# Kernel optimization log

Measured on AMD Instinct MI355X. Metric: run time of the kernel, lower is better.

## Reference

```python
import jax, jax.numpy as jnp
import numpy as np

B, T, D, H, L, O = 256, 512, 64, 256, 2, 4


def _lstm_layer(x_tbd, W_ih, W_hh, b_ih, b_hh):
    """x_tbd: (T, B, D_in) -> hidden sequence (T, B, H). PyTorch gate order i,f,g,o."""
    Bb = x_tbd.shape[1]
    Hh = W_hh.shape[1]
    b = b_ih + b_hh
    # precompute input projections for all timesteps in one GEMM
    xW = jnp.einsum('tbd,gd->tbg', x_tbd, W_ih) + b  # (T, B, 4H)

    def step(carry, xw_t):
        h, c = carry
        gates = xw_t + h @ W_hh.T
        i, f, g, o = jnp.split(gates, 4, axis=-1)
        i = jax.nn.sigmoid(i)
        f = jax.nn.sigmoid(f)
        g = jnp.tanh(g)
        o = jax.nn.sigmoid(o)
        c = f * c + i * g
        h = o * jnp.tanh(c)
        return (h, c), h

    init = (jnp.zeros((Bb, Hh), x_tbd.dtype), jnp.zeros((Bb, Hh), x_tbd.dtype))
    _, hs = jax.lax.scan(step, init, xW)
    return hs


def setup_inputs() -> dict:
    key = jax.random.key(0)
    ks = jax.random.split(key, 11)
    s = 1.0 / np.sqrt(H)  # PyTorch LSTM init scale
    inp = {
        'x': jax.random.normal(ks[0], (B, T, D), dtype=jnp.float32),
        'W_ih0': jax.random.uniform(ks[1], (4 * H, D), minval=-s, maxval=s, dtype=jnp.float32),
        'W_hh0': jax.random.uniform(ks[2], (4 * H, H), minval=-s, maxval=s, dtype=jnp.float32),
        'b_ih0': jax.random.uniform(ks[3], (4 * H,), minval=-s, maxval=s, dtype=jnp.float32),
        'b_hh0': jax.random.uniform(ks[4], (4 * H,), minval=-s, maxval=s, dtype=jnp.float32),
        'W_ih1': jax.random.uniform(ks[5], (4 * H, H), minval=-s, maxval=s, dtype=jnp.float32),
        'W_hh1': jax.random.uniform(ks[6], (4 * H, H), minval=-s, maxval=s, dtype=jnp.float32),
        'b_ih1': jax.random.uniform(ks[7], (4 * H,), minval=-s, maxval=s, dtype=jnp.float32),
        'b_hh1': jax.random.uniform(ks[8], (4 * H,), minval=-s, maxval=s, dtype=jnp.float32),
        'fc_W': jax.random.uniform(ks[9], (O, H), minval=-s, maxval=s, dtype=jnp.float32),
        'fc_b': jax.random.uniform(ks[10], (O,), minval=-s, maxval=s, dtype=jnp.float32),
    }
    return inp


def reference(x, W_ih0, W_hh0, b_ih0, b_hh0, W_ih1, W_hh1, b_ih1, b_hh1, fc_W, fc_b):
    xt = jnp.transpose(x, (1, 0, 2))            # (T, B, D), batch_first -> time-major
    h1 = _lstm_layer(xt, W_ih0, W_hh0, b_ih0, b_hh0)   # (T, B, H)
    h2 = _lstm_layer(h1, W_ih1, W_hh1, b_ih1, b_hh1)   # (T, B, H)
    last = h2[-1]                                # out[:, -1, :] in batch_first layout
    return last @ fc_W.T + fc_b                  # (B, O)
```

## Files before the change

### kernel.cpp

```cpp
#include <hip/hip_runtime.h>


#define TT 512
#define HH 256
#define DD 64

typedef __attribute__((ext_vector_type(2))) _Float16 h2t;
typedef __attribute__((ext_vector_type(8))) _Float16 f16x8;
typedef __attribute__((ext_vector_type(4))) float f32x4;
typedef unsigned long long u64;
typedef unsigned u32;

__device__ __forceinline__ u32 pkh(float x, float y) {
    h2t h; h.x = (_Float16)x; h.y = (_Float16)y;
    return __builtin_bit_cast(u32, h);
}
__device__ __forceinline__ float sigf(float x) { return 1.f / (1.f + __expf(-x)); }
__device__ __forceinline__ float tanhf_(float x) {
    float e = __expf(2.f * x);
    return 1.f - 2.f / (e + 1.f);
}
__device__ __forceinline__ f16x8 ld8(const float* p) {
    float4 u = ((const float4*)p)[0];
    float4 v = ((const float4*)p)[1];
    f16x8 r = {(_Float16)u.x, (_Float16)u.y, (_Float16)u.z, (_Float16)u.w,
               (_Float16)v.x, (_Float16)v.y, (_Float16)v.z, (_Float16)v.w};
    return r;
}
__device__ __forceinline__ u32 ld32(const u32* p) {
    return __hip_atomic_load(p, __ATOMIC_RELAXED, __HIP_MEMORY_SCOPE_AGENT);
}
__device__ __forceinline__ void st32(u32* p, u32 v) {
    __hip_atomic_store(p, v, __ATOMIC_RELAXED, __HIP_MEMORY_SCOPE_AGENT);
}
__device__ __forceinline__ u64 ld64(const u64* p) {
    return __hip_atomic_load(p, __ATOMIC_RELAXED, __HIP_MEMORY_SCOPE_AGENT);
}
__device__ __forceinline__ void st64(u64* p, u64 v) {
    __hip_atomic_store(p, v, __ATOMIC_RELAXED, __HIP_MEMORY_SCOPE_AGENT);
}

__global__ __launch_bounds__(512, 2) void lstm_persist(
    const float* __restrict__ x,
    const float* __restrict__ Wih0, const float* __restrict__ Whh0,
    const float* __restrict__ bih0, const float* __restrict__ bhh0,
    const float* __restrict__ Wih1, const float* __restrict__ Whh1,
    const float* __restrict__ bih1, const float* __restrict__ bhh1,
    const float* __restrict__ fcW, const float* __restrict__ fcb,
    float* __restrict__ out,
    u64* h0ring, u64* h1ring, u32* cflagsA)
{
    __shared__ __align__(16) _Float16 sB[9216];
    __shared__ __align__(16) float part2[2][8][276];

    const int tid  = threadIdx.x;
    const int g    = blockIdx.x & 31;
    const int role = blockIdx.x >> 5;
    const bool isL1 = role >= 4;
    const int q = role & 3;
    const int batch0 = g * 8;
    u64* ring0 = h0ring + (size_t)g * 4096;
    u64* ring1 = h1ring + (size_t)g * 4096;
    u32* cflag = cflagsA + (size_t)g * 16;

    const int lane = tid & 63, w = tid >> 6;
    const int mw = w & 3, kh = w >> 2;
    const int bcol = lane & 15, kc = lane >> 4;

    const int R0 = mw * 256 + 64 * q + (lane & 15);
    const int R1 = R0 + 16, R2 = R0 + 32, R3 = R0 + 48;

#define DECL_TI(ti) f16x8 A##ti##_0={},A##ti##_1={},A##ti##_2={},A##ti##_3={}, \
                          A##ti##_4={},A##ti##_5={},A##ti##_6={},A##ti##_7={};
    DECL_TI(0) DECL_TI(1) DECL_TI(2) DECL_TI(3)
#undef DECL_TI

    if (isL1) {
#define LDA1(ti,j) { int k_ = (kh*8+(j))*32 + kc*8;                          \
        A##ti##_##j = ld8(k_ < 256 ? Wih1 + (size_t)R##ti*256 + k_           \
                                   : Whh1 + (size_t)R##ti*256 + (k_-256)); }
#define LDA1T(ti) LDA1(ti,0) LDA1(ti,1) LDA1(ti,2) LDA1(ti,3) \
                  LDA1(ti,4) LDA1(ti,5) LDA1(ti,6) LDA1(ti,7)
        LDA1T(0) LDA1T(1) LDA1T(2) LDA1T(3)
#undef LDA1T
#undef LDA1
    } else {
#define LDA0(ti,j) { int k_ = (kh*5+(j))*32 + kc*8;                          \
        A##ti##_##j = ld8(k_ < 64 ? Wih0 + (size_t)R##ti*64 + k_             \
                                  : Whh0 + (size_t)R##ti*256 + (k_-64)); }
#define LDA0T(ti) LDA0(ti,0) LDA0(ti,1) LDA0(ti,2) LDA0(ti,3) LDA0(ti,4)
        LDA0T(0) LDA0T(1) LDA0T(2) LDA0T(3)
#undef LDA0T
#undef LDA0
    }

    const float* bA = isL1 ? bih1 : bih0;
    const float* bB = isL1 ? bhh1 : bhh0;
    const float bz0 = bA[      64*q + lane] + bB[      64*q + lane];
    const float bz1 = bA[256 + 64*q + lane] + bB[256 + 64*q + lane];
    const float bz2 = bA[512 + 64*q + lane] + bB[512 + 64*q + lane];
    const float bz3 = bA[768 + 64*q + lane] + bB[768 + 64*q + lane];
    float cst = 0.f;

    u32* const sBu = (u32*)sB;
    for (int i = tid; i < 4608; i += 512) sBu[i] = 0;

    auto stage_next = [&](int snext) {
        const bool st0 = (!isL1) && (snext < TT);
        const bool st1 = isL1 && (snext >= 1) && (snext <= TT);
        if (!(st0 || st1)) return;
        {
            const int slot = (snext - 1) & 3;
            const u32 e0 = (u32)snext;
            const int base = isL1 ? 0 : 8;
#pragma unroll
            for (int pp = 0; pp < 2; ++pp) {
                int p = tid + pp * 512;
                int j = p >> 7, n = p & 127;
                const u64* a = ring0 + slot * 1024 + (n >> 5) * 256 + j * 32 + (n & 31);
                u64 v;
                do { v = ld64(a); } while ((u32)(v >> 32) != e0);
                sBu[(base + (n >> 2)) * 72 + j * 4 + (n & 3)] = (u32)v;
            }
        }
        if (isL1) {
            const int slot = (snext + 2) & 3;
            const u32 e1 = (snext >= 2) ? (u32)snext : 0u;
#pragma unroll
            for (int pp = 0; pp < 2; ++pp) {
                int p = tid + pp * 512;
                int j = p >> 7, n = p & 127;
                const u64* a = ring1 + slot * 1024 + (n >> 5) * 256 + j * 32 + (n & 31);
                u64 v;
                do { v = ld64(a); } while ((u32)(v >> 32) != e1);
                sBu[(32 + (n >> 2)) * 72 + j * 4 + (n & 3)] = (u32)v;
            }
        } else if (tid >= 256 && tid < 384) {
            int t2 = tid - 256, j = t2 >> 4, c = t2 & 15;
            float4 v = ((const float4*)(x + ((size_t)(batch0 + j) * TT + snext) * DD))[c];
            int bidx = (c >> 1) * 72 + j * 4 + (c & 1) * 2;
            sBu[bidx]     = pkh(v.x, v.y);
            sBu[bidx + 1] = pkh(v.z, v.w);
        }
    };
    stage_next(0);

    for (int s = 0; s <= TT; ++s) {
        __syncthreads();
        if (tid == 0) st32(&cflag[role], (u32)(s + 1));

        const bool act_ = isL1 ? (s >= 1) : (s < TT);

        u32 cpre = 0xFFFFFFFFu;
        if (act_ && lane < 8) cpre = ld32(&cflag[lane]);

        if (act_) {
            f32x4 C0 = {0,0,0,0}, C1 = {0,0,0,0}, C2 = {0,0,0,0}, C3 = {0,0,0,0};
#define MST(j, ktb) { const f16x8 Bf = *(const f16x8*)(sB + (((ktb)+(j))*4 + kc)*144 + bcol*8); \
            C0 = __builtin_amdgcn_mfma_f32_16x16x32_f16(A0_##j, Bf, C0, 0,0,0); \
            C1 = __builtin_amdgcn_mfma_f32_16x16x32_f16(A1_##j, Bf, C1, 0,0,0); \
            C2 = __builtin_amdgcn_mfma_f32_16x16x32_f16(A2_##j, Bf, C2, 0,0,0); \
            C3 = __builtin_amdgcn_mfma_f32_16x16x32_f16(A3_##j, Bf, C3, 0,0,0); }
            if (isL1) {
                const int ktb = kh * 8;
                MST(0,ktb) MST(1,ktb) MST(2,ktb) MST(3,ktb)
                MST(4,ktb) MST(5,ktb) MST(6,ktb) MST(7,ktb)
            } else {
                const int ktb = kh * 5;
                MST(0,ktb) MST(1,ktb) MST(2,ktb) MST(3,ktb) MST(4,ktb)
            }
#undef MST
            if (bcol < 8) {
                *(f32x4*)&part2[kh][bcol][mw*64 +  0 + kc*4] = C0;
                *(f32x4*)&part2[kh][bcol][mw*64 + 16 + kc*4] = C1;
                *(f32x4*)&part2[kh][bcol][mw*64 + 32 + kc*4] = C2;
                *(f32x4*)&part2[kh][bcol][mw*64 + 48 + kc*4] = C3;
            }
        }
        __syncthreads();

        if (act_) {
            float s0 = part2[0][w][      lane] + part2[1][w][      lane] + bz0;
            float s1 = part2[0][w][ 64 + lane] + part2[1][w][ 64 + lane] + bz1;
            float s2 = part2[0][w][128 + lane] + part2[1][w][128 + lane] + bz2;
            float s3 = part2[0][w][192 + lane] + part2[1][w][192 + lane] + bz3;
            float fi = sigf(s0), ff = sigf(s1), fg = tanhf_(s2), fo = sigf(s3);
            cst = ff * cst + fi * fg;
            float h = fo * tanhf_(cst);
            float hn = __shfl_down(h, 1);

            const int tgt = s - 2;
            while (!__all(lane >= 8 || (int)cpre >= tgt)) {
                __builtin_amdgcn_s_sleep(1);
                if (lane < 8) cpre = ld32(&cflag[lane]);
            }
            if (!(lane & 1)) {
                u64 v = ((u64)(u32)(s + 1) << 32) | (u64)pkh(h, hn);
                u64* dst = (isL1 ? ring1 + (size_t)((s - 1) & 3) * 1024
                                 : ring0 + (size_t)(s & 3) * 1024)
                           + q * 256 + w * 32 + (lane >> 1);
                st64(dst, v);
            }
        }

        stage_next(s + 1);
    }

    if (isL1 && q == 0) {
        const u32 ef = (u32)(TT + 1);
#pragma unroll
        for (int pp = 0; pp < 2; ++pp) {
            int p = tid + pp * 512;
            int j = p >> 7, n = p & 127;
            const u64* a = ring1 + 3 * 1024 + (n >> 5) * 256 + j * 32 + (n & 31);
            u64 v;
            do { v = ld64(a); } while ((u32)(v >> 32) != ef);
            sBu[j * 128 + n] = (u32)v;
        }
        __syncthreads();
        const int j = tid >> 6, l2 = tid & 63;
        const int o = l2 >> 4, kk = l2 & 15;
        float ssum = 0.f;
#pragma unroll
        for (int m = 0; m < 16; ++m) {
            int k = kk * 16 + m;
            ssum += (float)sB[j * 256 + k] * fcW[o * HH + k];
        }
#pragma unroll
        for (int off = 8; off; off >>= 1) ssum += __shfl_down(ssum, off);
        if (kk == 0) out[(batch0 + j) * 4 + o] = ssum + fcb[o];
    }
}

extern "C" void kernel_launch(void* const* d_in, const int* in_sizes, int n_in,
                              void* d_out, int out_size, void* d_ws, size_t ws_size,
                              hipStream_t stream)
{
    (void)in_sizes; (void)n_in; (void)out_size; (void)ws_size;
    const float* x    = (const float*)d_in[0];
    const float* Wih0 = (const float*)d_in[1];
    const float* Whh0 = (const float*)d_in[2];
    const float* bih0 = (const float*)d_in[3];
    const float* bhh0 = (const float*)d_in[4];
    const float* Wih1 = (const float*)d_in[5];
    const float* Whh1 = (const float*)d_in[6];
    const float* bih1 = (const float*)d_in[7];
    const float* bhh1 = (const float*)d_in[8];
    const float* fcW  = (const float*)d_in[9];
    const float* fcb  = (const float*)d_in[10];
    float* out = (float*)d_out;

    u64* h0ring = (u64*)d_ws;
    u64* h1ring = (u64*)((char*)d_ws + 1048576);
    u32* cflags = (u32*)((char*)d_ws + 2097152);

    hipMemsetAsync(d_ws, 0, 2097152 + 2048, stream);

    lstm_persist<<<dim3(256), dim3(512), 0, stream>>>(
        x, Wih0, Whh0, bih0, bhh0, Wih1, Whh1, bih1, bhh1, fcW, fcb, out,
        h0ring, h1ring, cflags);
}
```

Measured before the change: 1.278 ms.

## Split input projections into separate producer blocks and pipeline them ahead of recurrence

```diff
diff --git a/kernel.cpp b/kernel.cpp
--- a/kernel.cpp
+++ b/kernel.cpp
@@ -39,6 +39,10 @@
 __device__ __forceinline__ void st64(u64* p, u64 v) {
     __hip_atomic_store(p, v, __ATOMIC_RELAXED, __HIP_MEMORY_SCOPE_AGENT);
 }
+
+#define MFMA16(A, B, C) __builtin_amdgcn_mfma_f32_16x16x32_f16((A), (B), (C), 0, 0, 0)
+
+#define DECLF(ti) f16x8 A##ti##_0 = {}, A##ti##_1 = {}, A##ti##_2 = {}, A##ti##_3 = {};
 
 __global__ __launch_bounds__(512, 2) void lstm_persist(
     const float* __restrict__ x,
@@ -48,187 +52,267 @@
     const float* __restrict__ bih1, const float* __restrict__ bhh1,
     const float* __restrict__ fcW, const float* __restrict__ fcb,
     float* __restrict__ out,
-    u64* h0ring, u64* h1ring, u32* cflagsA)
+    u64* wsu, u32* cflagsA)
 {
-    __shared__ __align__(16) _Float16 sB[9216];
-    __shared__ __align__(16) float part2[2][8][276];
+    __shared__ __align__(16) char ldsraw[9216 + 33280];
+    _Float16* const sB16 = (_Float16*)ldsraw;
+    u32* const sBu = (u32*)ldsraw;
+    float (*const part2)[8][520] = (float(*)[8][520])(ldsraw + 9216);
+    float (*const p1)[1032] = (float(*)[1032])(ldsraw + 9216);
 
     const int tid  = threadIdx.x;
     const int g    = blockIdx.x & 31;
     const int role = blockIdx.x >> 5;
-    const bool isL1 = role >= 4;
-    const int q = role & 3;
     const int batch0 = g * 8;
-    u64* ring0 = h0ring + (size_t)g * 4096;
-    u64* ring1 = h1ring + (size_t)g * 4096;
-    u32* cflag = cflagsA + (size_t)g * 16;
+    u64* const h0ring = wsu + (size_t)g * 4096;
+    u64* const h1ring = wsu + 131072 + (size_t)g * 4096;
+    u64* const u0ring = wsu + 262144 + (size_t)g * 16384;
+    u64* const u1ring = wsu + 786432 + (size_t)g * 16384;
+    u32* const cflag  = cflagsA + (size_t)g * 16;
 
     const int lane = tid & 63, w = tid >> 6;
     const int mw = w & 3, kh = w >> 2;
     const int bcol = lane & 15, kc = lane >> 4;
 
-    const int R0 = mw * 256 + 64 * q + (lane & 15);
-    const int R1 = R0 + 16, R2 = R0 + 32, R3 = R0 + 48;
-
-#define DECL_TI(ti) f16x8 A##ti##_0={},A##ti##_1={},A##ti##_2={},A##ti##_3={}, \
-                          A##ti##_4={},A##ti##_5={},A##ti##_6={},A##ti##_7={};
-    DECL_TI(0) DECL_TI(1) DECL_TI(2) DECL_TI(3)
-#undef DECL_TI
-
-    if (isL1) {
-#define LDA1(ti,j) { int k_ = (kh*8+(j))*32 + kc*8;                          \
-        A##ti##_##j = ld8(k_ < 256 ? Wih1 + (size_t)R##ti*256 + k_           \
-                                   : Whh1 + (size_t)R##ti*256 + (k_-256)); }
-#define LDA1T(ti) LDA1(ti,0) LDA1(ti,1) LDA1(ti,2) LDA1(ti,3) \
-                  LDA1(ti,4) LDA1(ti,5) LDA1(ti,6) LDA1(ti,7)
-        LDA1T(0) LDA1T(1) LDA1T(2) LDA1T(3)
-#undef LDA1T
-#undef LDA1
+    for (int i = tid; i < 2304; i += 512) sBu[i] = 0;
+    __syncthreads();
+
+    if (role < 4) {
+        const int hf = role & 1;
+        const bool L1 = role >= 2;
+        const float* const W = L1 ? Whh1 : Whh0;
+        u64* const hring = L1 ? h1ring : h0ring;
+        const u64* const uring = L1 ? u1ring : u0ring;
+        const int ng = L1 ? 1 : 3;
+        const int gfi = (lane == 0) ? (role ^ 1) : (3 + lane);
+
+        DECLF(0) DECLF(1) DECLF(2) DECLF(3) DECLF(4) DECLF(5) DECLF(6) DECLF(7)
+#define LREC(ti) { const int R_ = mw * 256 + hf * 128 + (ti) * 16 + (lane & 15);  \
+        const float* rw_ = W + (size_t)R_ * 256 + kh * 128 + kc * 8;              \
+        A##ti##_0 = ld8(rw_);      A##ti##_1 = ld8(rw_ + 32);                     \
+        A##ti##_2 = ld8(rw_ + 64); A##ti##_3 = ld8(rw_ + 96); }
+        LREC(0) LREC(1) LREC(2) LREC(3) LREC(4) LREC(5) LREC(6) LREC(7)
+#undef LREC
+
+        const int j2 = w;
+        const int up = lane;
+        float c0_ = 0.f, c1_ = 0.f;
+
+        for (int s = 0; s < TT; ++s) {
+            if (tid == 0) st32(&cflag[role], (u32)(s + 1));
+            u32 cp = 0;
+            if (lane < ng) cp = ld32(&cflag[gfi]);
+
+            {
+                const f16x8 B0_ = *(const f16x8*)(sB16 + (kh*16 + 0*4 + kc)*144 + bcol*8);
+                const f16x8 B1_ = *(const f16x8*)(sB16 + (kh*16 + 1*4 + kc)*144 + bcol*8);
+                const f16x8 B2_ = *(const f16x8*)(sB16 + (kh*16 + 2*4 + kc)*144 + bcol*8);
+                const f16x8 B3_ = *(const f16x8*)(sB16 + (kh*16 + 3*4 + kc)*144 + bcol*8);
+#define MTR(ti) { f32x4 C_ = {0,0,0,0};                                           \
+                C_ = MFMA16(A##ti##_0, B0_, C_); C_ = MFMA16(A##ti##_1, B1_, C_); \
+                C_ = MFMA16(A##ti##_2, B2_, C_); C_ = MFMA16(A##ti##_3, B3_, C_); \
+                if (bcol < 8)                                                     \
+                    *(f32x4*)&part2[kh][bcol][mw*128 + (ti)*16 + kc*4] = C_; }
+                MTR(0) MTR(1) MTR(2) MTR(3) MTR(4) MTR(5) MTR(6) MTR(7)
+#undef MTR
+            }
+            __syncthreads();
+
+            const u32 eu = (u32)(s + 1);
+            const u64* ub_ = uring + (size_t)(s & 3) * 4096 + (size_t)j2 * 512
+                             + hf * 64 + up;
+            const u64 *ua0 = ub_, *ua1 = ub_ + 128, *ua2 = ub_ + 256, *ua3 = ub_ + 384;
+            u64 v0 = ld64(ua0), v1 = ld64(ua1), v2 = ld64(ua2), v3 = ld64(ua3);
+            for (;;) {
+                bool k0 = ((u32)(v0 >> 32) == eu), k1 = ((u32)(v1 >> 32) == eu);
+                bool k2 = ((u32)(v2 >> 32) == eu), k3 = ((u32)(v3 >> 32) == eu);
+                if (k0 & k1 & k2 & k3) break;
+                if (!k0) v0 = ld64(ua0);
+                if (!k1) v1 = ld64(ua1);
+                if (!k2) v2 = ld64(ua2);
+                if (!k3) v3 = ld64(ua3);
+            }
+            float e0, o0, e1, o1, e2, o2, e3, o3;
+#define GG(gi, vv) { const float2 xa = *(const float2*)&part2[0][j2][(gi)*128 + 2*up]; \
+            const float2 xb = *(const float2*)&part2[1][j2][(gi)*128 + 2*up];          \
+            const h2t uh = __builtin_bit_cast(h2t, (u32)(vv));                         \
+            e##gi = xa.x + xb.x + (float)uh.x; o##gi = xa.y + xb.y + (float)uh.y; }
+            GG(0, v0) GG(1, v1) GG(2, v2) GG(3, v3)
+#undef GG
+            {
+                float ie = sigf(e0), fe = sigf(e1), ge = tanhf_(e2), oe = sigf(e3);
+                c0_ = fe * c0_ + ie * ge;
+                e0 = oe * tanhf_(c0_);
+            }
+            {
+                float io = sigf(o0), fo = sigf(o1), go = tanhf_(o2), oo = sigf(o3);
+                c1_ = fo * c1_ + io * go;
+                o0 = oo * tanhf_(c1_);
+            }
+            const u32 hw = pkh(e0, o0);
+
+            sBu[(hf*16 + (up >> 2)) * 72 + j2 * 4 + (up & 3)] = hw;
+
+            {
+                const int tgt = s - 2;
+                while (!__all(lane >= ng || (int)cp >= tgt)) {
+                    __builtin_amdgcn_s_sleep(1);
+                    if (lane < ng) cp = ld32(&cflag[gfi]);
+                }
+            }
+            st64(hring + (size_t)(s & 3) * 1024 + (size_t)hf * 512 + j2 * 64 + up,
+                 ((u64)eu << 32) | (u64)hw);
+
+            {
+                const u64* pa_ = hring + (size_t)(s & 3) * 1024
+                                 + (size_t)(1 - hf) * 512 + j2 * 64 + up;
+                u64 pv = ld64(pa_);
+                while ((u32)(pv >> 32) != eu) pv = ld64(pa_);
+                sBu[((1 - hf)*16 + (up >> 2)) * 72 + j2 * 4 + (up & 3)] = (u32)pv;
+            }
+            __syncthreads();
+        }
+
+        if (role == 2) {
+            const int j = tid >> 6, l2 = tid & 63;
+            const int o = l2 >> 4, kk = l2 & 15;
+            float ssum = 0.f;
+#pragma unroll
+            for (int m = 0; m < 16; ++m) {
+                int k = kk * 16 + m;
+                ssum += (float)sB16[(k >> 3) * 144 + j * 8 + (k & 7)] * fcW[o * HH + k];
+            }
+#pragma unroll
+            for (int off = 8; off; off >>= 1) ssum += __shfl_down(ssum, off);
+            if (kk == 0) out[(batch0 + j) * 4 + o] = ssum + fcb[o];
+        }
+    } else if (role < 6) {
+        const int rh = role - 4;
+        DECLF(0) DECLF(1) DECLF(2) DECLF(3) DECLF(4) DECLF(5) DECLF(6) DECLF(7)
+#define LU1(ti) { const int R_ = rh * 512 + mw * 128 + (ti) * 16 + (lane & 15);   \
+        const float* rw_ = Wih1 + (size_t)R_ * 256 + kh * 128 + kc * 8;           \
+        A##ti##_0 = ld8(rw_);      A##ti##_1 = ld8(rw_ + 32);                     \
+        A##ti##_2 = ld8(rw_ + 64); A##ti##_3 = ld8(rw_ + 96); }
+        LU1(0) LU1(1) LU1(2) LU1(3) LU1(4) LU1(5) LU1(6) LU1(7)
+#undef LU1
+        float bA0, bA1, bB0, bB1, bC0, bC1, bD0, bD1;
+        {
+            int r;
+            r = rh*512 + 2*(lane +   0); bA0 = bih1[r] + bhh1[r]; bA1 = bih1[r+1] + bhh1[r+1];
+            r = rh*512 + 2*(lane +  64); bB0 = bih1[r] + bhh1[r]; bB1 = bih1[r+1] + bhh1[r+1];
+            r = rh*512 + 2*(lane + 128); bC0 = bih1[r] + bhh1[r]; bC1 = bih1[r+1] + bhh1[r+1];
+            r = rh*512 + 2*(lane + 192); bD0 = bih1[r] + bhh1[r]; bD1 = bih1[r+1] + bhh1[r+1];
+        }
+
+        for (int s = 0; s < TT; ++s) {
+            if (tid == 0) st32(&cflag[role], (u32)(s + 1));
+            u32 cp = 0;
+            if (lane < 2) cp = ld32(&cflag[2 + lane]);
+
+            const u32 eu = (u32)(s + 1);
+            {
+                const u64* hb = h0ring + (size_t)(s & 3) * 1024;
+                const u64 *a0 = hb + tid, *a1 = hb + 512 + tid;
+                u64 v0 = ld64(a0), v1 = ld64(a1);
+                for (;;) {
+                    bool k0 = ((u32)(v0 >> 32) == eu), k1 = ((u32)(v1 >> 32) == eu);
+                    if (k0 & k1) break;
+                    if (!k0) v0 = ld64(a0);
+                    if (!k1) v1 = ld64(a1);
+                }
+                const int jj = (tid >> 6) & 7, uu = tid & 63;
+                sBu[(     (uu >> 2)) * 72 + jj * 4 + (uu & 3)] = (u32)v0;
+                sBu[(16 + (uu >> 2)) * 72 + jj * 4 + (uu & 3)] = (u32)v1;
+            }
+            __syncthreads();
+
+            {
+                const f16x8 B0_ = *(const f16x8*)(sB16 + (kh*16 + 0*4 + kc)*144 + bcol*8);
+                const f16x8 B1_ = *(const f16x8*)(sB16 + (kh*16 + 1*4 + kc)*144 + bcol*8);
+                const f16x8 B2_ = *(const f16x8*)(sB16 + (kh*16 + 2*4 + kc)*144 + bcol*8);
+                const f16x8 B3_ = *(const f16x8*)(sB16 + (kh*16 + 3*4 + kc)*144 + bcol*8);
+#define MTR(ti) { f32x4 C_ = {0,0,0,0};                                           \
+                C_ = MFMA16(A##ti##_0, B0_, C_); C_ = MFMA16(A##ti##_1, B1_, C_); \
+                C_ = MFMA16(A##ti##_2, B2_, C_); C_ = MFMA16(A##ti##_3, B3_, C_); \
+                if (bcol < 8)                                                     \
+                    *(f32x4*)&part2[kh][bcol][mw*128 + (ti)*16 + kc*4] = C_; }
+                MTR(0) MTR(1) MTR(2) MTR(3) MTR(4) MTR(5) MTR(6) MTR(7)
+#undef MTR
+            }
+            __syncthreads();
+
+            {
+                const int tgt = s - 2;
+                while (!__all(lane >= 2 || (int)cp >= tgt)) {
+                    __builtin_amdgcn_s_sleep(1);
+                    if (lane < 2) cp = ld32(&cflag[2 + lane]);
+                }
+            }
+            {
+                const u64 ep = (u64)eu << 32;
+                u64* ubst = u1ring + (size_t)(s & 3) * 4096 + (size_t)w * 512 + rh * 256;
+#define STU(kk_, bz0n, bz1n) { const int rp_ = lane + 64*(kk_); const int r0_ = 2*rp_; \
+                float lo_ = part2[0][w][r0_] + part2[1][w][r0_] + bz0n;                \
+                float hi_ = part2[0][w][r0_ + 1] + part2[1][w][r0_ + 1] + bz1n;        \
+                st64(ubst + rp_, ep | (u64)pkh(lo_, hi_)); }
+                STU(0, bA0, bA1) STU(1, bB0, bB1) STU(2, bC0, bC1) STU(3, bD0, bD1)
+#undef STU
+            }
+        }
     } else {
-#define LDA0(ti,j) { int k_ = (kh*5+(j))*32 + kc*8;                          \
-        A##ti##_##j = ld8(k_ < 64 ? Wih0 + (size_t)R##ti*64 + k_             \
-                                  : Whh0 + (size_t)R##ti*256 + (k_-64)); }
-#define LDA0T(ti) LDA0(ti,0) LDA0(ti,1) LDA0(ti,2) LDA0(ti,3) LDA0(ti,4)
-        LDA0T(0) LDA0T(1) LDA0T(2) LDA0T(3)
-#undef LDA0T
-#undef LDA0
-    }
-
-    const float* bA = isL1 ? bih1 : bih0;
-    const float* bB = isL1 ? bhh1 : bhh0;
-    const float bz0 = bA[      64*q + lane] + bB[      64*q + lane];
-    const float bz1 = bA[256 + 64*q + lane] + bB[256 + 64*q + lane];
-    const float bz2 = bA[512 + 64*q + lane] + bB[512 + 64*q + lane];
-    const float bz3 = bA[768 + 64*q + lane] + bB[768 + 64*q + lane];
-    float cst = 0.f;
-
-    u32* const sBu = (u32*)sB;
-    for (int i = tid; i < 4608; i += 512) sBu[i] = 0;
-
-    auto stage_next = [&](int snext) {
-        const bool st0 = (!isL1) && (snext < TT);
-        const bool st1 = isL1 && (snext >= 1) && (snext <= TT);
-        if (!(st0 || st1)) return;
-        {
-            const int slot = (snext - 1) & 3;
-            const u32 e0 = (u32)snext;
-            const int base = isL1 ? 0 : 8;
+        DECLF(0) DECLF(1) DECLF(2) DECLF(3) DECLF(4) DECLF(5) DECLF(6) DECLF(7)
+#define LU0(ti) { const int R_ = w * 128 + (ti) * 16 + (lane & 15);               \
+        const float* rw_ = Wih0 + (size_t)R_ * 64 + kc * 8;                       \
+        A##ti##_0 = ld8(rw_); A##ti##_1 = ld8(rw_ + 32); }
+        LU0(0) LU0(1) LU0(2) LU0(3) LU0(4) LU0(5) LU0(6) LU0(7)
+#undef LU0
+
+        for (int s = 0; s < TT; ++s) {
+            if (tid == 0) st32(&cflag[role], (u32)(s + 1));
+            u32 cp = 0;
+            if (lane < 2) cp = ld32(&cflag[lane]);
+
+            if (tid < 128) {
+                const int j = tid >> 4, c = tid & 15;
+                const float4 v = *(const float4*)(
+                    x + ((size_t)(batch0 + j) * TT + s) * DD + c * 4);
+                const int bi = (c >> 1) * 72 + j * 4 + (c & 1) * 2;
+                sBu[bi]     = pkh(v.x, v.y);
+                sBu[bi + 1] = pkh(v.z, v.w);
+            }
+            __syncthreads();
+
+            {
+                const f16x8 B0_ = *(const f16x8*)(sB16 + kc * 144 + bcol * 8);
+                const f16x8 B1_ = *(const f16x8*)(sB16 + (4 + kc) * 144 + bcol * 8);
+#define MT0(ti) { f32x4 C_ = {0,0,0,0};                                           \
+                C_ = MFMA16(A##ti##_0, B0_, C_); C_ = MFMA16(A##ti##_1, B1_, C_); \
+                if (bcol < 8)                                                     \
+                    *(f32x4*)&p1[bcol][w*128 + (ti)*16 + kc*4] = C_; }
+                MT0(0) MT0(1) MT0(2) MT0(3) MT0(4) MT0(5) MT0(6) MT0(7)
+#undef MT0
+            }
+            __syncthreads();
+
+            {
+                const int tgt = s - 2;
+                while (!__all(lane >= 2 || (int)cp >= tgt)) {
+                    __builtin_amdgcn_s_sleep(1);
+                    if (lane < 2) cp = ld32(&cflag[lane]);
+                }
+            }
+            {
+                const u64 ep = (u64)(u32)(s + 1) << 32;
+                u64* ubst = u0ring + (size_t)(s & 3) * 4096 + (size_t)w * 512;
 #pragma unroll
-            for (int pp = 0; pp < 2; ++pp) {
-                int p = tid + pp * 512;
-                int j = p >> 7, n = p & 127;
-                const u64* a = ring0 + slot * 1024 + (n >> 5) * 256 + j * 32 + (n & 31);
-                u64 v;
-                do { v = ld64(a); } while ((u32)(v >> 32) != e0);
-                sBu[(base + (n >> 2)) * 72 + j * 4 + (n & 3)] = (u32)v;
-            }
-        }
-        if (isL1) {
-            const int slot = (snext + 2) & 3;
-            const u32 e1 = (snext >= 2) ? (u32)snext : 0u;
-#pragma unroll
-            for (int pp = 0; pp < 2; ++pp) {
-                int p = tid + pp * 512;
-                int j = p >> 7, n = p & 127;
-                const u64* a = ring1 + slot * 1024 + (n >> 5) * 256 + j * 32 + (n & 31);
-                u64 v;
-                do { v = ld64(a); } while ((u32)(v >> 32) != e1);
-                sBu[(32 + (n >> 2)) * 72 + j * 4 + (n & 3)] = (u32)v;
-            }
-        } else if (tid >= 256 && tid < 384) {
-            int t2 = tid - 256, j = t2 >> 4, c = t2 & 15;
-            float4 v = ((const float4*)(x + ((size_t)(batch0 + j) * TT + snext) * DD))[c];
-            int bidx = (c >> 1) * 72 + j * 4 + (c & 1) * 2;
-            sBu[bidx]     = pkh(v.x, v.y);
-            sBu[bidx + 1] = pkh(v.z, v.w);
-        }
-    };
-    stage_next(0);
-
-    for (int s = 0; s <= TT; ++s) {
-        __syncthreads();
-        if (tid == 0) st32(&cflag[role], (u32)(s + 1));
-
-        const bool act_ = isL1 ? (s >= 1) : (s < TT);
-
-        u32 cpre = 0xFFFFFFFFu;
-        if (act_ && lane < 8) cpre = ld32(&cflag[lane]);
-
-        if (act_) {
-            f32x4 C0 = {0,0,0,0}, C1 = {0,0,0,0}, C2 = {0,0,0,0}, C3 = {0,0,0,0};
-#define MST(j, ktb) { const f16x8 Bf = *(const f16x8*)(sB + (((ktb)+(j))*4 + kc)*144 + bcol*8); \
-            C0 = __builtin_amdgcn_mfma_f32_16x16x32_f16(A0_##j, Bf, C0, 0,0,0); \
-            C1 = __builtin_amdgcn_mfma_f32_16x16x32_f16(A1_##j, Bf, C1, 0,0,0); \
-            C2 = __builtin_amdgcn_mfma_f32_16x16x32_f16(A2_##j, Bf, C2, 0,0,0); \
-            C3 = __builtin_amdgcn_mfma_f32_16x16x32_f16(A3_##j, Bf, C3, 0,0,0); }
-            if (isL1) {
-                const int ktb = kh * 8;
-                MST(0,ktb) MST(1,ktb) MST(2,ktb) MST(3,ktb)
-                MST(4,ktb) MST(5,ktb) MST(6,ktb) MST(7,ktb)
-            } else {
-                const int ktb = kh * 5;
-                MST(0,ktb) MST(1,ktb) MST(2,ktb) MST(3,ktb) MST(4,ktb)
-            }
-#undef MST
-            if (bcol < 8) {
-                *(f32x4*)&part2[kh][bcol][mw*64 +  0 + kc*4] = C0;
-                *(f32x4*)&part2[kh][bcol][mw*64 + 16 + kc*4] = C1;
-                *(f32x4*)&part2[kh][bcol][mw*64 + 32 + kc*4] = C2;
-                *(f32x4*)&part2[kh][bcol][mw*64 + 48 + kc*4] = C3;
-            }
-        }
-        __syncthreads();
-
-        if (act_) {
-            float s0 = part2[0][w][      lane] + part2[1][w][      lane] + bz0;
-            float s1 = part2[0][w][ 64 + lane] + part2[1][w][ 64 + lane] + bz1;
-            float s2 = part2[0][w][128 + lane] + part2[1][w][128 + lane] + bz2;
-            float s3 = part2[0][w][192 + lane] + part2[1][w][192 + lane] + bz3;
-            float fi = sigf(s0), ff = sigf(s1), fg = tanhf_(s2), fo = sigf(s3);
-            cst = ff * cst + fi * fg;
-            float h = fo * tanhf_(cst);
-            float hn = __shfl_down(h, 1);
-
-            const int tgt = s - 2;
-            while (!__all(lane >= 8 || (int)cpre >= tgt)) {
-                __builtin_amdgcn_s_sleep(1);
-                if (lane < 8) cpre = ld32(&cflag[lane]);
-            }
-            if (!(lane & 1)) {
-                u64 v = ((u64)(u32)(s + 1) << 32) | (u64)pkh(h, hn);
-                u64* dst = (isL1 ? ring1 + (size_t)((s - 1) & 3) * 1024
-                                 : ring0 + (size_t)(s & 3) * 1024)
-                           + q * 256 + w * 32 + (lane >> 1);
-                st64(dst, v);
-            }
-        }
-
-        stage_next(s + 1);
-    }
-
-    if (isL1 && q == 0) {
-        const u32 ef = (u32)(TT + 1);
-#pragma unroll
-        for (int pp = 0; pp < 2; ++pp) {
-            int p = tid + pp * 512;
-            int j = p >> 7, n = p & 127;
-            const u64* a = ring1 + 3 * 1024 + (n >> 5) * 256 + j * 32 + (n & 31);
-            u64 v;
-            do { v = ld64(a); } while ((u32)(v >> 32) != ef);
-            sBu[j * 128 + n] = (u32)v;
-        }
-        __syncthreads();
-        const int j = tid >> 6, l2 = tid & 63;
-        const int o = l2 >> 4, kk = l2 & 15;
-        float ssum = 0.f;
-#pragma unroll
-        for (int m = 0; m < 16; ++m) {
-            int k = kk * 16 + m;
-            ssum += (float)sB[j * 256 + k] * fcW[o * HH + k];
-        }
-#pragma unroll
-        for (int off = 8; off; off >>= 1) ssum += __shfl_down(ssum, off);
-        if (kk == 0) out[(batch0 + j) * 4 + o] = ssum + fcb[o];
+                for (int k = 0; k < 8; ++k) {
+                    const int rp = lane + 64 * k, r0 = 2 * rp;
+                    const float lo = p1[w][r0] + bih0[r0] + bhh0[r0];
+                    const float hi = p1[w][r0 + 1] + bih0[r0 + 1] + bhh0[r0 + 1];
+                    st64(ubst + rp, ep | (u64)pkh(lo, hi));
+                }
+            }
+        }
     }
 }
 
@@ -250,13 +334,12 @@
     const float* fcb  = (const float*)d_in[10];
     float* out = (float*)d_out;
 
-    u64* h0ring = (u64*)d_ws;
-    u64* h1ring = (u64*)((char*)d_ws + 1048576);
-    u32* cflags = (u32*)((char*)d_ws + 2097152);
-
-    hipMemsetAsync(d_ws, 0, 2097152 + 2048, stream);
-
-    lstm_persist<<<dim3(256), dim3(512), 0, stream>>>(
+    u64* wsu    = (u64*)d_ws;
+    u32* cflags = (u32*)((char*)d_ws + 10485760);
+
+    hipMemsetAsync(d_ws, 0, 10485760 + 2048, stream);
+
+    lstm_persist<<<dim3(224), dim3(512), 0, stream>>>(
         x, Wih0, Whh0, bih0, bhh0, Wih1, Whh1, bih1, bhh1, fcW, fcb, out,
-        h0ring, h1ring, cflags);
-}
+        wsu, cflags);
+}
```

New measurement: 1.572 ms. +23.0%, slower.
